# Performance work log

Measured on AMD Instinct MI355X. Metric: run time of the kernel, lower is better.

The kernel has to match this reference:

```python
import jax, jax.numpy as jnp
import numpy as np

N_NODES = 100000


def spmm(edge_src, edge_dst, edge_w, h):
    # out[d] = sum_{e: dst[e]=d} w[e] * h[src[e]]  -- sparse adj @ h
    return jax.ops.segment_sum(h[edge_src] * edge_w[:, None], edge_dst,
                               num_segments=N_NODES)


def gcn_layer(x, W, edge_src, edge_dst, edge_w, use_activation):
    support = x @ W                      # dense projection [N, out]
    out = spmm(edge_src, edge_dst, edge_w, support)
    return jax.nn.relu(out) if use_activation else out


def setup_inputs() -> dict:
    key = jax.random.key(0)
    ks = jax.random.split(key, 9)
    n_edges = 3200000

    def xavier(k, shape):
        fan_in, fan_out = shape
        a = jnp.sqrt(6.0 / (fan_in + fan_out))
        return jax.random.uniform(k, shape, jnp.float32, -a, a)

    return {
        "x": jax.random.normal(ks[0], (N_NODES, 512), jnp.float32),
        "edge_src": jax.random.randint(ks[1], (n_edges,), 0, N_NODES, jnp.int32),
        "edge_dst": jax.random.randint(ks[2], (n_edges,), 0, N_NODES, jnp.int32),
        "edge_w": jax.random.uniform(ks[3], (n_edges,), jnp.float32),
        "W1": xavier(ks[4], (512, 128)),
        "W2": xavier(ks[5], (128, 64)),
        "W3": xavier(ks[6], (64, 32)),
        "Wmu": xavier(ks[7], (32, 16)),
        "Wlv": xavier(ks[8], (32, 16)),
    }


def reference(x, edge_src, edge_dst, edge_w, W1, W2, W3, Wmu, Wlv):
    # Eval-mode GCNVAE forward: dropout is identity, z = mu.
    h1 = gcn_layer(x, W1, edge_src, edge_dst, edge_w, True)
    h2 = gcn_layer(h1, W2, edge_src, edge_dst, edge_w, True)
    h3 = gcn_layer(h2, W3, edge_src, edge_dst, edge_w, True)
    mu = gcn_layer(h3, Wmu, edge_src, edge_dst, edge_w, False)
    logvar = gcn_layer(h3, Wlv, edge_src, edge_dst, edge_w, False)
    z = mu  # reparameterize in eval mode returns mu
    return (z, mu, logvar)
```

## Files before the change

### kernel.cpp

```cpp
#include <hip/hip_runtime.h>

typedef __attribute__((ext_vector_type(4))) float floatx4;
typedef __attribute__((ext_vector_type(8))) short bf16x8;

#define NPB 256
#define CHUNK 6144
#define MAXB 12288

__device__ __forceinline__ float bf2f(unsigned short h) {
  union { unsigned int u; float f; } c; c.u = ((unsigned int)h) << 16; return c.f;
}
__device__ __forceinline__ unsigned short f2bf(float f) {
  union { float f; unsigned int u; } c; c.f = f;
  unsigned int r = c.u + 0x7FFFu + ((c.u >> 16) & 1u);
  return (unsigned short)(r >> 16);
}

__device__ __forceinline__ void gl16(const void* g, void* l) {
  __builtin_amdgcn_global_load_lds(
      (const __attribute__((address_space(1))) unsigned int*)g,
      (__attribute__((address_space(3))) unsigned int*)l, 16, 0, 0);
}


__global__ __launch_bounds__(256) void bhist_k(const int* __restrict__ dst,
                                               int* __restrict__ bcnt, int E, int B) {
  __shared__ int h[512];
  int tid = threadIdx.x;
  for (int i = tid; i < 512; i += 256) h[i] = 0;
  __syncthreads();
  for (int i = blockIdx.x * 256 + tid; i < E; i += gridDim.x * 256)
    atomicAdd(&h[dst[i] >> 8], 1);
  __syncthreads();
  for (int i = tid; i < B; i += 256)
    if (h[i]) atomicAdd(&bcnt[i], h[i]);
}

__global__ __launch_bounds__(512) void bscan_k(const int* __restrict__ bcnt,
                                               int* __restrict__ bstart,
                                               int* __restrict__ bcur, int B) {
  __shared__ int s[512];
  int tid = threadIdx.x;
  int v = (tid < B) ? bcnt[tid] : 0;
  s[tid] = v;
  __syncthreads();
  for (int off = 1; off < 512; off <<= 1) {
    int t = (tid >= off) ? s[tid - off] : 0;
    __syncthreads();
    s[tid] += t;
    __syncthreads();
  }
  int excl = s[tid] - v;
  if (tid < B) { bstart[tid] = excl; bcur[tid] = excl; }
  if (tid == 511) bstart[B] = s[511];
}

__global__ __launch_bounds__(256) void part_k(const int* __restrict__ src,
                                              const int* __restrict__ dst,
                                              const float* __restrict__ w,
                                              int* __restrict__ bcur,
                                              int2* __restrict__ prec, int E, int B) {
  __shared__ int hist[512];
  __shared__ int lstart[512];
  __shared__ int cur[512];
  __shared__ int gbase[512];
  __shared__ int ss[256];
  __shared__ int2 srt[CHUNK];
  int tid = threadIdx.x;
  int e0 = blockIdx.x * CHUNK;
  int cnt = min(CHUNK, E - e0);
  for (int i = tid; i < 512; i += 256) hist[i] = 0;
  __syncthreads();
  for (int i = tid; i < cnt; i += 256) atomicAdd(&hist[dst[e0 + i] >> 8], 1);
  __syncthreads();
  int a0 = hist[2 * tid], a1 = hist[2 * tid + 1];
  ss[tid] = a0 + a1;
  __syncthreads();
  for (int off = 1; off < 256; off <<= 1) {
    int t = (tid >= off) ? ss[tid - off] : 0;
    __syncthreads();
    ss[tid] += t;
    __syncthreads();
  }
  int excl = tid ? ss[tid - 1] : 0;
  lstart[2 * tid] = excl;     cur[2 * tid] = excl;
  lstart[2 * tid + 1] = excl + a0; cur[2 * tid + 1] = excl + a0;
  __syncthreads();
  for (int i = tid; i < B; i += 256)
    gbase[i] = hist[i] ? atomicAdd(&bcur[i], hist[i]) : 0;
  __syncthreads();
  for (int i = tid; i < cnt; i += 256) {
    int d = dst[e0 + i];
    int b = d >> 8;
    float wf = w[e0 + i];
    int w15 = (int)(wf * 32768.f + 0.5f);
    if (w15 > 32767) w15 = 32767;
    int2 r;
    r.x = src[e0 + i] | (w15 << 17);
    r.y = (b << 8) | (d & 255);
    int pos = atomicAdd(&cur[b], 1);
    srt[pos] = r;
  }
  __syncthreads();
  for (int j = tid; j < cnt; j += 256) {
    int2 r = srt[j];
    int b = r.y >> 8;
    prec[gbase[b] + (j - lstart[b])] = make_int2(r.x, r.y & 255);
  }
}

__global__ __launch_bounds__(256) void sort_k(const int2* __restrict__ prec,
                                              const int* __restrict__ bstart,
                                              unsigned int* __restrict__ recs,
                                              int* __restrict__ row_start,
                                              int* __restrict__ counts, int N, int B) {
  __shared__ int hist[256], lstart[256], cur[256], ss[256];
  __shared__ unsigned int srt[MAXB];
  int b = blockIdx.x;
  int tid = threadIdx.x;
  int s = bstart[b];
  int cnt = bstart[b + 1] - s;
  if (cnt > MAXB) cnt = MAXB;
  hist[tid] = 0;
  __syncthreads();
  for (int i = tid; i < cnt; i += 256) atomicAdd(&hist[prec[s + i].y], 1);
  __syncthreads();
  ss[tid] = hist[tid];
  __syncthreads();
  for (int off = 1; off < 256; off <<= 1) {
    int t = (tid >= off) ? ss[tid - off] : 0;
    __syncthreads();
    ss[tid] += t;
    __syncthreads();
  }
  int excl = ss[tid] - hist[tid];
  lstart[tid] = excl;
  cur[tid] = excl;
  int node = b * NPB + tid;
  if (node < N) { row_start[node] = s + excl; counts[node] = hist[tid]; }
  __syncthreads();
  for (int i = tid; i < cnt; i += 256) {
    int2 r = prec[s + i];
    int pos = atomicAdd(&cur[r.y], 1);
    srt[pos] = (unsigned int)r.x;
  }
  __syncthreads();
  for (int i = tid; i < cnt; i += 256) recs[s + i] = srt[i];
}


__global__ __launch_bounds__(256) void tw1_k(const float* __restrict__ W1,
                                             unsigned short* __restrict__ W1t) {
  int i = blockIdx.x * 256 + threadIdx.x;
  if (i >= 512 * 128) return;
  int k = i >> 7, n = i & 127;
  W1t[n * 512 + k] = f2bf(W1[i]);
}


__device__ __forceinline__ bf16x8 cvt8(float4 lo, float4 hi) {
  bf16x8 r;
  r[0] = (short)f2bf(lo.x); r[1] = (short)f2bf(lo.y);
  r[2] = (short)f2bf(lo.z); r[3] = (short)f2bf(lo.w);
  r[4] = (short)f2bf(hi.x); r[5] = (short)f2bf(hi.y);
  r[6] = (short)f2bf(hi.z); r[7] = (short)f2bf(hi.w);
  return r;
}

__global__ __launch_bounds__(256, 3) void gemm1_mfma(const float* __restrict__ A,
                                                     const unsigned short* __restrict__ W1t,
                                                     unsigned short* __restrict__ C, int N) {
  constexpr int BK = 32;
  __shared__ __align__(16) float          As[2][128 * BK];
  __shared__ __align__(16) unsigned short Bs[2][128 * BK];
  int tid = threadIdx.x;
  int lane = tid & 63;
  int w = tid >> 6;
  int m0 = lane & 15;
  int kq = lane >> 4;
  int rowBase = blockIdx.x * 128;

  floatx4 acc[8][2];
#pragma unroll
  for (int i = 0; i < 8; ++i)
#pragma unroll
    for (int j = 0; j < 2; ++j) acc[i][j] = (floatx4)0.f;

  size_t aSrc[4]; int aDst[4];
#pragma unroll
  for (int it = 0; it < 4; ++it) {
    int c = it * 256 + w * 64 + lane;
    int r = c >> 3, ch = c & 7;
    int sc = ch ^ (r & 7);
    int gr = rowBase + r;
    if (gr > N - 1) gr = N - 1;
    aSrc[it] = (size_t)gr * 512 + sc * 4;
    aDst[it] = (it * 256 + w * 64) * 4;
  }
  size_t bSrc[2]; int bDst[2];
#pragma unroll
  for (int it = 0; it < 2; ++it) {
    int c = it * 256 + w * 64 + lane;
    int n = c >> 2, ch = c & 3;
    bSrc[it] = (size_t)n * 512 + ch * 8;
    bDst[it] = (it * 256 + w * 64) * 8;
  }

  auto stage = [&](int bi, int k0) {
#pragma unroll
    for (int it = 0; it < 4; ++it) gl16(&A[aSrc[it] + k0], &As[bi][aDst[it]]);
#pragma unroll
    for (int it = 0; it < 2; ++it) gl16(&W1t[bSrc[it] + k0], &Bs[bi][bDst[it]]);
  };

  stage(0, 0);
  int cur = 0;
  for (int t = 0; t < 16; ++t) {
    if (t < 15) {
      stage(cur ^ 1, (t + 1) * BK);
      asm volatile("s_waitcnt vmcnt(6)" ::: "memory");
    } else {
      asm volatile("s_waitcnt vmcnt(0)" ::: "memory");
    }
    __builtin_amdgcn_s_barrier();

    bf16x8 bb0 = *reinterpret_cast<const bf16x8*>(&Bs[cur][(w * 32 + m0) * BK + kq * 8]);
    bf16x8 bb1 = *reinterpret_cast<const bf16x8*>(&Bs[cur][(w * 32 + 16 + m0) * BK + kq * 8]);
#pragma unroll
    for (int mi = 0; mi < 8; ++mi) {
      int row = mi * 16 + m0;
      int s = row & 7;
      float4 lo = *reinterpret_cast<const float4*>(&As[cur][row * BK + (((2 * kq) ^ s) << 2)]);
      float4 hi = *reinterpret_cast<const float4*>(&As[cur][row * BK + (((2 * kq + 1) ^ s) << 2)]);
      bf16x8 a = cvt8(lo, hi);
      acc[mi][0] = __builtin_amdgcn_mfma_f32_16x16x32_bf16(a, bb0, acc[mi][0], 0, 0, 0);
      acc[mi][1] = __builtin_amdgcn_mfma_f32_16x16x32_bf16(a, bb1, acc[mi][1], 0, 0, 0);
    }
    __builtin_amdgcn_s_barrier();
    cur ^= 1;
  }

#pragma unroll
  for (int mi = 0; mi < 8; ++mi) {
#pragma unroll
    for (int jn = 0; jn < 2; ++jn) {
      int gc = w * 32 + jn * 16 + m0;
#pragma unroll
      for (int p = 0; p < 4; ++p) {
        int gr = rowBase + mi * 16 + kq * 4 + p;
        if (gr < N) C[(size_t)gr * 128 + gc] = f2bf(acc[mi][jn][p]);
      }
    }
  }
}


template <int K, int O>
__global__ __launch_bounds__(256) void gemm_kernel(const unsigned short* __restrict__ A,
                                                   const float* __restrict__ W,
                                                   unsigned short* __restrict__ C, int N) {
  constexpr int BM = 64;
  constexpr int BK = 32;
  constexpr int TM = 4;
  constexpr int TN = O / 16;
  __shared__ float As[BK][BM];
  __shared__ float Ws[BK][O];
  int tid = threadIdx.x;
  int tx = tid % 16;
  int ty = tid / 16;
  int rowBase = blockIdx.x * BM;
  float acc[TM][TN];
#pragma unroll
  for (int i = 0; i < TM; ++i)
#pragma unroll
    for (int j = 0; j < TN; ++j) acc[i][j] = 0.f;

  for (int k0 = 0; k0 < K; k0 += BK) {
    {
      int r = tid >> 2;
      int kc = (tid & 3) * 8;
      int gr = rowBase + r;
      uint4 v = make_uint4(0u, 0u, 0u, 0u);
      if (gr < N) v = *reinterpret_cast<const uint4*>(&A[(size_t)gr * K + k0 + kc]);
      const unsigned short* pv = reinterpret_cast<const unsigned short*>(&v);
#pragma unroll
      for (int j = 0; j < 8; ++j) As[kc + j][r] = bf2f(pv[j]);
    }
    {
      constexpr int ELEMS = BK * O / 256;
      constexpr int NV = ELEMS / 4;
#pragma unroll
      for (int it = 0; it < NV; ++it) {
        int linear = (tid + it * 256) * 4;
        int kk = linear / O;
        int oo = linear % O;
        float4 v = *reinterpret_cast<const float4*>(&W[(size_t)(k0 + kk) * O + oo]);
        Ws[kk][oo + 0] = v.x; Ws[kk][oo + 1] = v.y;
        Ws[kk][oo + 2] = v.z; Ws[kk][oo + 3] = v.w;
      }
    }
    __syncthreads();
#pragma unroll
    for (int k = 0; k < BK; ++k) {
      float a[TM], w[TN];
#pragma unroll
      for (int i = 0; i < TM; ++i) a[i] = As[k][ty * TM + i];
#pragma unroll
      for (int j = 0; j < TN; ++j) w[j] = Ws[k][tx * TN + j];
#pragma unroll
      for (int i = 0; i < TM; ++i)
#pragma unroll
        for (int j = 0; j < TN; ++j) acc[i][j] += a[i] * w[j];
    }
    __syncthreads();
  }
#pragma unroll
  for (int i = 0; i < TM; ++i) {
    int gr = rowBase + ty * TM + i;
    if (gr >= N) continue;
#pragma unroll
    for (int j = 0; j < TN; j += 2) {
      unsigned int p = ((unsigned int)f2bf(acc[i][j + 1]) << 16) | f2bf(acc[i][j]);
      *reinterpret_cast<unsigned int*>(&C[(size_t)gr * O + tx * TN + j]) = p;
    }
  }
}


#define INV32768 3.0517578125e-05f

template <int O, bool RELU>
__global__ __launch_bounds__(256) void spmm_kernel(const unsigned int* __restrict__ recs,
                                                   const int* __restrict__ row_start,
                                                   const int* __restrict__ counts,
                                                   const unsigned short* __restrict__ sup,
                                                   unsigned short* __restrict__ hout, int N) {
  constexpr int SUBW = O / 2;
  constexpr int NPW = 256 / SUBW;
  constexpr int U = 8;
  int tid = threadIdx.x;
  int lane = tid % SUBW;
  int sub = tid / SUBW;
  int node = blockIdx.x * NPW + sub;
  if (node >= N) return;
  int start = row_start[node];
  int deg = counts[node];
  const unsigned int* supu = reinterpret_cast<const unsigned int*>(sup);
  const unsigned int* rp = recs + start;
  float a0 = 0.f, a1 = 0.f;
  int i = 0;
  for (; i + U <= deg; i += U) {
    unsigned int r[U];
#pragma unroll
    for (int j = 0; j < U; ++j) r[j] = rp[i + j];
    unsigned int v[U];
#pragma unroll
    for (int j = 0; j < U; ++j) v[j] = supu[(size_t)(r[j] & 0x1FFFFu) * (O / 2) + lane];
#pragma unroll
    for (int j = 0; j < U; ++j) {
      float w = (float)(r[j] >> 17) * INV32768;
      a0 += w * bf2f((unsigned short)(v[j] & 0xFFFFu));
      a1 += w * bf2f((unsigned short)(v[j] >> 16));
    }
  }
  for (; i < deg; ++i) {
    unsigned int rec = rp[i];
    float w = (float)(rec >> 17) * INV32768;
    unsigned int v = supu[(size_t)(rec & 0x1FFFFu) * (O / 2) + lane];
    a0 += w * bf2f((unsigned short)(v & 0xFFFFu));
    a1 += w * bf2f((unsigned short)(v >> 16));
  }
  if (RELU) { a0 = fmaxf(a0, 0.f); a1 = fmaxf(a1, 0.f); }
  unsigned int p = ((unsigned int)f2bf(a1) << 16) | f2bf(a0);
  reinterpret_cast<unsigned int*>(hout)[(size_t)node * (O / 2) + lane] = p;
}

__global__ __launch_bounds__(256) void spmm_mulv_kernel(const unsigned int* __restrict__ recs,
                                                        const int* __restrict__ row_start,
                                                        const int* __restrict__ counts,
                                                        const unsigned short* __restrict__ sup,
                                                        float* __restrict__ out, int N) {
  constexpr int SUBW = 16;
  constexpr int NPW = 256 / SUBW;
  constexpr int U = 8;
  int tid = threadIdx.x;
  int lane = tid % SUBW;
  int sub = tid / SUBW;
  int node = blockIdx.x * NPW + sub;
  if (node >= N) return;
  int start = row_start[node];
  int deg = counts[node];
  const unsigned int* supu = reinterpret_cast<const unsigned int*>(sup);
  const unsigned int* rp = recs + start;
  float a0 = 0.f, a1 = 0.f;
  int i = 0;
  for (; i + U <= deg; i += U) {
    unsigned int r[U];
#pragma unroll
    for (int j = 0; j < U; ++j) r[j] = rp[i + j];
    unsigned int v[U];
#pragma unroll
    for (int j = 0; j < U; ++j) v[j] = supu[(size_t)(r[j] & 0x1FFFFu) * 16 + lane];
#pragma unroll
    for (int j = 0; j < U; ++j) {
      float w = (float)(r[j] >> 17) * INV32768;
      a0 += w * bf2f((unsigned short)(v[j] & 0xFFFFu));
      a1 += w * bf2f((unsigned short)(v[j] >> 16));
    }
  }
  for (; i < deg; ++i) {
    unsigned int rec = rp[i];
    float w = (float)(rec >> 17) * INV32768;
    unsigned int v = supu[(size_t)(rec & 0x1FFFFu) * 16 + lane];
    a0 += w * bf2f((unsigned short)(v & 0xFFFFu));
    a1 += w * bf2f((unsigned short)(v >> 16));
  }
  size_t nf = (size_t)N * 16;
  if (lane < 8) {
    float2 p = make_float2(a0, a1);
    *reinterpret_cast<float2*>(&out[(size_t)node * 16 + lane * 2]) = p;
    *reinterpret_cast<float2*>(&out[nf + (size_t)node * 16 + lane * 2]) = p;
  } else {
    int l = lane - 8;
    *reinterpret_cast<float2*>(&out[2 * nf + (size_t)node * 16 + l * 2]) =
        make_float2(a0, a1);
  }
}

__global__ void packw_k(const float* __restrict__ Wmu,
                        const float* __restrict__ Wlv,
                        float* __restrict__ Wcat) {
  int i = blockIdx.x * 256 + threadIdx.x;
  if (i >= 32 * 32) return;
  int k = i / 32, o = i % 32;
  Wcat[i] = (o < 16) ? Wmu[k * 16 + o] : Wlv[k * 16 + (o - 16)];
}


extern "C" void kernel_launch(void* const* d_in, const int* in_sizes, int n_in,
                              void* d_out, int out_size, void* d_ws, size_t ws_size,
                              hipStream_t stream) {
  const float* x    = (const float*)d_in[0];
  const int* esrc   = (const int*)d_in[1];
  const int* edst   = (const int*)d_in[2];
  const float* ew   = (const float*)d_in[3];
  const float* W1   = (const float*)d_in[4];
  const float* W2   = (const float*)d_in[5];
  const float* W3   = (const float*)d_in[6];
  const float* Wmu  = (const float*)d_in[7];
  const float* Wlv  = (const float*)d_in[8];
  float* out = (float*)d_out;
  int N = in_sizes[0] / 512;
  int E = in_sizes[1];
  int B = (N + NPB - 1) / NPB;

  char* p = (char*)d_ws;
  auto alloc = [&](size_t bytes) -> char* {
    char* r = p;
    p += (bytes + 255) & ~(size_t)255;
    return r;
  };
  int*  counts = (int*)alloc((size_t)N * 4);
  int*  rowst  = (int*)alloc((size_t)N * 4);
  int*  bcnt   = (int*)alloc((size_t)(B + 1) * 4);
  int*  bstart = (int*)alloc((size_t)(B + 1) * 4);
  int*  bcur   = (int*)alloc((size_t)(B + 1) * 4);
  int2* prec   = (int2*)alloc((size_t)E * 8);
  unsigned int* recs = (unsigned int*)alloc((size_t)E * 4);
  unsigned short* bufA = (unsigned short*)alloc((size_t)N * 128 * 2);
  unsigned short* bufB = (unsigned short*)alloc((size_t)N * 128 * 2);
  unsigned short* W1t  = (unsigned short*)alloc(512 * 128 * 2);
  float* Wcat = (float*)alloc(32 * 32 * 4);

  hipMemsetAsync(bcnt, 0, (size_t)(B + 1) * 4, stream);
  bhist_k<<<256, 256, 0, stream>>>(edst, bcnt, E, B);
  bscan_k<<<1, 512, 0, stream>>>(bcnt, bstart, bcur, B);
  part_k<<<(E + CHUNK - 1) / CHUNK, 256, 0, stream>>>(esrc, edst, ew, bcur, prec, E, B);
  sort_k<<<B, 256, 0, stream>>>(prec, bstart, recs, rowst, counts, N, B);

  tw1_k<<<256, 256, 0, stream>>>(W1, W1t);
  gemm1_mfma<<<(N + 127) / 128, 256, 0, stream>>>(x, W1t, bufA, N);
  spmm_kernel<128, true><<<(N + 3) / 4, 256, 0, stream>>>(recs, rowst, counts, bufA, bufB, N);

  int gemmGrid = (N + 63) / 64;

  gemm_kernel<128, 64><<<gemmGrid, 256, 0, stream>>>(bufB, W2, bufA, N);
  spmm_kernel<64, true><<<(N + 7) / 8, 256, 0, stream>>>(recs, rowst, counts, bufA, bufB, N);

  gemm_kernel<64, 32><<<gemmGrid, 256, 0, stream>>>(bufB, W3, bufA, N);
  spmm_kernel<32, true><<<(N + 15) / 16, 256, 0, stream>>>(recs, rowst, counts, bufA, bufB, N);

  packw_k<<<4, 256, 0, stream>>>(Wmu, Wlv, Wcat);
  gemm_kernel<32, 32><<<gemmGrid, 256, 0, stream>>>(bufB, Wcat, bufA, N);
  spmm_mulv_kernel<<<(N + 15) / 16, 256, 0, stream>>>(recs, rowst, counts, bufA, out, N);
}
```

Baseline: 770.2 us.

## Store GEMM outputs in 16-column slices and run SpMM per slice

GEMM kernels now write their support matrix as column slices of 16 bf16 values, each slice contiguous over nodes. The SpMM kernels launch one block per (node group, slice), with 8 lanes per node gathering 32-byte rows. This shrinks the gather working set per slice, which should give better L2 reuse of the random source rows. It also adds nontemporal loads and stores and folds the remainder loop into a predicated main loop. The trade-off is that edge records are re-read once per slice and the number of blocks grows.

```diff
diff --git a/kernel.cpp b/kernel.cpp
--- a/kernel.cpp
+++ b/kernel.cpp
@@ -245,10 +245,12 @@
 #pragma unroll
     for (int jn = 0; jn < 2; ++jn) {
       int gc = w * 32 + jn * 16 + m0;
+      int sl = gc >> 4, cl = gc & 15;
+      size_t base = (size_t)sl * N * 16 + cl;
 #pragma unroll
       for (int p = 0; p < 4; ++p) {
         int gr = rowBase + mi * 16 + kq * 4 + p;
-        if (gr < N) C[(size_t)gr * 128 + gc] = f2bf(acc[mi][jn][p]);
+        if (gr < N) C[base + (size_t)gr * 16] = f2bf(acc[mi][jn][p]);
       }
     }
   }
@@ -321,7 +323,9 @@
 #pragma unroll
     for (int j = 0; j < TN; j += 2) {
       unsigned int p = ((unsigned int)f2bf(acc[i][j + 1]) << 16) | f2bf(acc[i][j]);
-      *reinterpret_cast<unsigned int*>(&C[(size_t)gr * O + tx * TN + j]) = p;
+      int gc = tx * TN + j;
+      *reinterpret_cast<unsigned int*>(
+          &C[(size_t)(gc >> 4) * N * 16 + (size_t)gr * 16 + (gc & 15)]) = p;
     }
   }
 }
@@ -329,33 +333,34 @@
 
 #define INV32768 3.0517578125e-05f
 
-template <int O, bool RELU>
-__global__ __launch_bounds__(256) void spmm_kernel(const unsigned int* __restrict__ recs,
-                                                   const int* __restrict__ row_start,
-                                                   const int* __restrict__ counts,
-                                                   const unsigned short* __restrict__ sup,
-                                                   unsigned short* __restrict__ hout, int N) {
-  constexpr int SUBW = O / 2;
-  constexpr int NPW = 256 / SUBW;
+template <int NSLICE, int OTOT, bool RELU>
+__global__ __launch_bounds__(256) void spmm_sl(const unsigned int* __restrict__ recs,
+                                               const int* __restrict__ row_start,
+                                               const int* __restrict__ counts,
+                                               const unsigned short* __restrict__ sup,
+                                               unsigned short* __restrict__ hout, int N) {
   constexpr int U = 8;
-  int tid = threadIdx.x;
-  int lane = tid % SUBW;
-  int sub = tid / SUBW;
-  int node = blockIdx.x * NPW + sub;
+  int slice = blockIdx.x % NSLICE;
+  int group = blockIdx.x / NSLICE;
+  int tid = threadIdx.x;
+  int lane = tid & 7;
+  int sub = tid >> 3;
+  int node = group * 32 + sub;
   if (node >= N) return;
   int start = row_start[node];
   int deg = counts[node];
-  const unsigned int* supu = reinterpret_cast<const unsigned int*>(sup);
+  const unsigned int* supu =
+      reinterpret_cast<const unsigned int*>(sup) + (size_t)slice * N * 8;
   const unsigned int* rp = recs + start;
   float a0 = 0.f, a1 = 0.f;
-  int i = 0;
-  for (; i + U <= deg; i += U) {
+  for (int i = 0; i < deg; i += U) {
     unsigned int r[U];
 #pragma unroll
-    for (int j = 0; j < U; ++j) r[j] = rp[i + j];
+    for (int j = 0; j < U; ++j)
+      r[j] = (i + j < deg) ? __builtin_nontemporal_load(&rp[i + j]) : 0u;
     unsigned int v[U];
 #pragma unroll
-    for (int j = 0; j < U; ++j) v[j] = supu[(size_t)(r[j] & 0x1FFFFu) * (O / 2) + lane];
+    for (int j = 0; j < U; ++j) v[j] = supu[((r[j] & 0x1FFFFu) << 3) + lane];
 #pragma unroll
     for (int j = 0; j < U; ++j) {
       float w = (float)(r[j] >> 17) * INV32768;
@@ -363,44 +368,39 @@
       a1 += w * bf2f((unsigned short)(v[j] >> 16));
     }
   }
-  for (; i < deg; ++i) {
-    unsigned int rec = rp[i];
-    float w = (float)(rec >> 17) * INV32768;
-    unsigned int v = supu[(size_t)(rec & 0x1FFFFu) * (O / 2) + lane];
-    a0 += w * bf2f((unsigned short)(v & 0xFFFFu));
-    a1 += w * bf2f((unsigned short)(v >> 16));
-  }
   if (RELU) { a0 = fmaxf(a0, 0.f); a1 = fmaxf(a1, 0.f); }
   unsigned int p = ((unsigned int)f2bf(a1) << 16) | f2bf(a0);
-  reinterpret_cast<unsigned int*>(hout)[(size_t)node * (O / 2) + lane] = p;
-}
-
-__global__ __launch_bounds__(256) void spmm_mulv_kernel(const unsigned int* __restrict__ recs,
-                                                        const int* __restrict__ row_start,
-                                                        const int* __restrict__ counts,
-                                                        const unsigned short* __restrict__ sup,
-                                                        float* __restrict__ out, int N) {
-  constexpr int SUBW = 16;
-  constexpr int NPW = 256 / SUBW;
+  __builtin_nontemporal_store(
+      p, reinterpret_cast<unsigned int*>(hout) + (size_t)node * (OTOT / 2) + slice * 8 + lane);
+}
+
+__global__ __launch_bounds__(256) void spmm_mulv_sl(const unsigned int* __restrict__ recs,
+                                                    const int* __restrict__ row_start,
+                                                    const int* __restrict__ counts,
+                                                    const unsigned short* __restrict__ sup,
+                                                    float* __restrict__ out, int N) {
   constexpr int U = 8;
-  int tid = threadIdx.x;
-  int lane = tid % SUBW;
-  int sub = tid / SUBW;
-  int node = blockIdx.x * NPW + sub;
+  int slice = blockIdx.x & 1;
+  int group = blockIdx.x >> 1;
+  int tid = threadIdx.x;
+  int lane = tid & 7;
+  int sub = tid >> 3;
+  int node = group * 32 + sub;
   if (node >= N) return;
   int start = row_start[node];
   int deg = counts[node];
-  const unsigned int* supu = reinterpret_cast<const unsigned int*>(sup);
+  const unsigned int* supu =
+      reinterpret_cast<const unsigned int*>(sup) + (size_t)slice * N * 8;
   const unsigned int* rp = recs + start;
   float a0 = 0.f, a1 = 0.f;
-  int i = 0;
-  for (; i + U <= deg; i += U) {
+  for (int i = 0; i < deg; i += U) {
     unsigned int r[U];
 #pragma unroll
-    for (int j = 0; j < U; ++j) r[j] = rp[i + j];
+    for (int j = 0; j < U; ++j)
+      r[j] = (i + j < deg) ? __builtin_nontemporal_load(&rp[i + j]) : 0u;
     unsigned int v[U];
 #pragma unroll
-    for (int j = 0; j < U; ++j) v[j] = supu[(size_t)(r[j] & 0x1FFFFu) * 16 + lane];
+    for (int j = 0; j < U; ++j) v[j] = supu[((r[j] & 0x1FFFFu) << 3) + lane];
 #pragma unroll
     for (int j = 0; j < U; ++j) {
       float w = (float)(r[j] >> 17) * INV32768;
@@ -408,22 +408,15 @@
       a1 += w * bf2f((unsigned short)(v[j] >> 16));
     }
   }
-  for (; i < deg; ++i) {
-    unsigned int rec = rp[i];
-    float w = (float)(rec >> 17) * INV32768;
-    unsigned int v = supu[(size_t)(rec & 0x1FFFFu) * 16 + lane];
-    a0 += w * bf2f((unsigned short)(v & 0xFFFFu));
-    a1 += w * bf2f((unsigned short)(v >> 16));
-  }
+  union { float f[2]; unsigned long long u; } pk;
+  pk.f[0] = a0; pk.f[1] = a1;
   size_t nf = (size_t)N * 16;
-  if (lane < 8) {
-    float2 p = make_float2(a0, a1);
-    *reinterpret_cast<float2*>(&out[(size_t)node * 16 + lane * 2]) = p;
-    *reinterpret_cast<float2*>(&out[nf + (size_t)node * 16 + lane * 2]) = p;
+  size_t o = (size_t)node * 16 + lane * 2;
+  if (slice == 0) {
+    __builtin_nontemporal_store(pk.u, reinterpret_cast<unsigned long long*>(out + o));
+    __builtin_nontemporal_store(pk.u, reinterpret_cast<unsigned long long*>(out + nf + o));
   } else {
-    int l = lane - 8;
-    *reinterpret_cast<float2*>(&out[2 * nf + (size_t)node * 16 + l * 2]) =
-        make_float2(a0, a1);
+    __builtin_nontemporal_store(pk.u, reinterpret_cast<unsigned long long*>(out + 2 * nf + o));
   }
 }
 
@@ -478,19 +471,21 @@
   part_k<<<(E + CHUNK - 1) / CHUNK, 256, 0, stream>>>(esrc, edst, ew, bcur, prec, E, B);
   sort_k<<<B, 256, 0, stream>>>(prec, bstart, recs, rowst, counts, N, B);
 
+  int ngroups = (N + 31) / 32;
+
   tw1_k<<<256, 256, 0, stream>>>(W1, W1t);
   gemm1_mfma<<<(N + 127) / 128, 256, 0, stream>>>(x, W1t, bufA, N);
-  spmm_kernel<128, true><<<(N + 3) / 4, 256, 0, stream>>>(recs, rowst, counts, bufA, bufB, N);
+  spmm_sl<8, 128, true><<<ngroups * 8, 256, 0, stream>>>(recs, rowst, counts, bufA, bufB, N);
 
   int gemmGrid = (N + 63) / 64;
 
   gemm_kernel<128, 64><<<gemmGrid, 256, 0, stream>>>(bufB, W2, bufA, N);
-  spmm_kernel<64, true><<<(N + 7) / 8, 256, 0, stream>>>(recs, rowst, counts, bufA, bufB, N);
+  spmm_sl<4, 64, true><<<ngroups * 4, 256, 0, stream>>>(recs, rowst, counts, bufA, bufB, N);
 
   gemm_kernel<64, 32><<<gemmGrid, 256, 0, stream>>>(bufB, W3, bufA, N);
-  spmm_kernel<32, true><<<(N + 15) / 16, 256, 0, stream>>>(recs, rowst, counts, bufA, bufB, N);
+  spmm_sl<2, 32, true><<<ngroups * 2, 256, 0, stream>>>(recs, rowst, counts, bufA, bufB, N);
 
   packw_k<<<4, 256, 0, stream>>>(Wmu, Wlv, Wcat);
   gemm_kernel<32, 32><<<gemmGrid, 256, 0, stream>>>(bufB, Wcat, bufA, N);
-  spmm_mulv_kernel<<<(N + 15) / 16, 256, 0, stream>>>(recs, rowst, counts, bufA, out, N);
-}
+  spmm_mulv_sl<<<ngroups * 2, 256, 0, stream>>>(recs, rowst, counts, bufA, out, N);
+}
```

New measurement: 1.244 ms. 1.62x slower.
